# Kernel tuning notes

Measured on AMD Instinct MI355X. Metric: run time of the kernel, lower is better.

## Reference

```python
import jax, jax.numpy as jnp
import numpy as np

B, T, D = 4, 2048, 1024
H = 16
HD = D // H  # 64


def setup_inputs() -> dict:
    key = jax.random.key(0)
    ks = jax.random.split(key, 7)
    scale = 1.0 / np.sqrt(D)
    x = jax.random.normal(ks[0], (B, T, D), dtype=jnp.float32)
    # per-head projection weights, stacked over heads: [H, D, HD]
    Wq = jax.random.normal(ks[1], (H, D, HD), dtype=jnp.float32) * scale
    Wk = jax.random.normal(ks[2], (H, D, HD), dtype=jnp.float32) * scale
    Wv = jax.random.normal(ks[3], (H, D, HD), dtype=jnp.float32) * scale
    s_raw = jnp.zeros((H,), dtype=jnp.float32)  # learnable ssmax scale per head
    proj_W = jax.random.normal(ks[4], (D, D), dtype=jnp.float32) * scale
    proj_b = jax.random.normal(ks[5], (D,), dtype=jnp.float32) * 0.01
    return {"x": x, "Wq": Wq, "Wk": Wk, "Wv": Wv, "s_raw": s_raw,
            "proj_W": proj_W, "proj_b": proj_b}


def reference(x, Wq, Wk, Wv, s_raw, proj_W, proj_b):
    # per-head q/k/v: [B, H, T, HD]
    q = jnp.einsum('btd,hde->bhte', x, Wq)
    k = jnp.einsum('btd,hde->bhte', x, Wk)
    v = jnp.einsum('btd,hde->bhte', x, Wv)

    # ssmax: q scaled by softplus(s) * log(position index, 1-based)
    logn = jnp.log(jnp.arange(1, T + 1, dtype=x.dtype))  # [T]
    s = jax.nn.softplus(s_raw)  # [H]
    q = q * (s[None, :, None, None] * logn[None, None, :, None])

    scores = jnp.einsum('bhte,bhse->bhts', q, k) * (HD ** -0.5)
    causal = jnp.tril(jnp.ones((T, T), dtype=bool))
    scores = jnp.where(causal[None, None], scores, -jnp.inf)
    w = jax.nn.softmax(scores, axis=-1)

    out = jnp.einsum('bhts,bhse->bhte', w, v)          # [B, H, T, HD]
    out = out.transpose(0, 2, 1, 3).reshape(B, T, D)    # concat heads
    return out @ proj_W.T + proj_b
```

## Files before the change

kernel.cpp:

```cpp
#include <hip/hip_runtime.h>
#include <hip/hip_bf16.h>

#define Bv 4
#define Tv 2048
#define Dv 1024
#define Hv 16
#define HDv 64
#define Mv (Bv*Tv)

typedef __hip_bfloat16 bf16;
typedef short s8v __attribute__((ext_vector_type(8)));
typedef float f4v __attribute__((ext_vector_type(4)));
typedef float f16a __attribute__((ext_vector_type(16)));

__device__ __forceinline__ unsigned short f2us(float x){
    bf16 h = __float2bfloat16(x);
    return *reinterpret_cast<unsigned short*>(&h);
}
__device__ __forceinline__ unsigned int pack2(float a, float b){
    return (unsigned int)f2us(a) | ((unsigned int)f2us(b) << 16);
}

__global__ void cvt_kernel(const float* __restrict__ src,
                           unsigned short* __restrict__ dst, int n4) {
    int i = blockIdx.x * 256 + threadIdx.x;
    if (i < n4) {
        float4 f = *(const float4*)(src + (size_t)i * 4);
        ushort4 o;
        o.x = f2us(f.x); o.y = f2us(f.y); o.z = f2us(f.z); o.w = f2us(f.w);
        *(ushort4*)(dst + (size_t)i * 4) = o;
    }
}

__global__ __launch_bounds__(256) void wt_kernel(
    const float* __restrict__ Wq, const float* __restrict__ Wk,
    const float* __restrict__ Wv, unsigned short* __restrict__ Wt)
{
    const int dt  = blockIdx.x;
    const int h   = blockIdx.y;
    const int sel = blockIdx.z;
    const float* W = (sel == 0) ? Wq : ((sel == 1) ? Wk : Wv);
    const float* Wh = W + (size_t)h * Dv * HDv;
    __shared__ float Tf[64][65];
    const int tid = threadIdx.x;
    for (int l = 0; l < 16; ++l) {
        int idx = tid + l * 256;
        int r = idx >> 6, e = idx & 63;
        Tf[r][e] = Wh[(size_t)(dt * 64 + r) * HDv + e];
    }
    __syncthreads();
    unsigned short* out = Wt + ((size_t)sel * Hv + h) * HDv * Dv;
    for (int l = 0; l < 16; ++l) {
        int idx = tid + l * 256;
        int e = idx >> 6, d = idx & 63;
        out[(size_t)e * Dv + dt * 64 + d] = f2us(Tf[d][e]);
    }
}

__global__ __launch_bounds__(256) void qkv_big(
    const unsigned short* __restrict__ xb, const unsigned short* __restrict__ Wc,
    const float* __restrict__ s_raw,
    unsigned short* __restrict__ q, unsigned short* __restrict__ k,
    unsigned short* __restrict__ vT)
{
    const int bm = blockIdx.x;
    const int bn = blockIdx.y;
    const int tid = threadIdx.x;
    const int w = tid >> 6, lane = tid & 63;
    const int n16 = lane & 15, quad = lane >> 4;
    const int wm = w >> 1, wn = w & 1;

    __shared__ __align__(16) unsigned short As[128][72];
    __shared__ __align__(16) unsigned short Bs[128][72];

    f4v acc[4][4];
    f4v zero = {0.f, 0.f, 0.f, 0.f};
    #pragma unroll
    for (int i = 0; i < 4; ++i)
        #pragma unroll
        for (int j = 0; j < 4; ++j) acc[i][j] = zero;

    const int row0 = bm * 128, col0 = bn * 128;

    for (int k0 = 0; k0 < Dv; k0 += 64) {
        __syncthreads();
        #pragma unroll
        for (int l = 0; l < 4; ++l) {
            int idx = tid + l * 256;
            int r = idx >> 3, g = idx & 7;
            *(ulonglong2*)(&As[r][g * 8]) =
                *(const ulonglong2*)(xb + (size_t)(row0 + r) * Dv + k0 + g * 8);
            *(ulonglong2*)(&Bs[r][g * 8]) =
                *(const ulonglong2*)(Wc + (size_t)(col0 + r) * Dv + k0 + g * 8);
        }
        __syncthreads();
        #pragma unroll
        for (int ks = 0; ks < 2; ++ks) {
            s8v bfr[4];
            #pragma unroll
            for (int ni = 0; ni < 4; ++ni)
                bfr[ni] = *(const s8v*)(&Bs[wn * 64 + ni * 16 + n16][ks * 32 + quad * 8]);
            #pragma unroll
            for (int mi = 0; mi < 4; ++mi) {
                s8v afr = *(const s8v*)(&As[wm * 64 + mi * 16 + n16][ks * 32 + quad * 8]);
                #pragma unroll
                for (int ni = 0; ni < 4; ++ni)
                    acc[mi][ni] = __builtin_amdgcn_mfma_f32_16x16x32_bf16(afr, bfr[ni], acc[mi][ni], 0, 0, 0);
            }
        }
    }

    #pragma unroll
    for (int ni = 0; ni < 4; ++ni) {
        int n = col0 + wn * 64 + ni * 16 + n16;
        int sel = n >> 10, h = (n >> 6) & 15, e = n & 63;
        if (sel == 2) {
            #pragma unroll
            for (int mi = 0; mi < 4; ++mi) {
                int row = row0 + wm * 64 + mi * 16 + quad * 4;
                int bb_ = row >> 11, t = row & (Tv - 1);
                ushort4 o4;
                o4.x = f2us(acc[mi][ni][0]); o4.y = f2us(acc[mi][ni][1]);
                o4.z = f2us(acc[mi][ni][2]); o4.w = f2us(acc[mi][ni][3]);
                *(ushort4*)(vT + ((size_t)(bb_ * Hv + h) * HDv + e) * Tv + t) = o4;
            }
        } else {
            unsigned short* out = (sel == 0) ? q : k;
            float sc_h = (sel == 0) ? log1pf(expf(s_raw[h])) * 0.125f : 1.0f;
            #pragma unroll
            for (int mi = 0; mi < 4; ++mi) {
                #pragma unroll
                for (int r = 0; r < 4; ++r) {
                    int row = row0 + wm * 64 + mi * 16 + quad * 4 + r;
                    int bb_ = row >> 11, t = row & (Tv - 1);
                    float rs = (sel == 0) ? sc_h * logf((float)(t + 1)) : 1.0f;
                    out[((size_t)(bb_ * Hv + h) * Tv + t) * HDv + e] = f2us(acc[mi][ni][r] * rs);
                }
            }
        }
    }
}

__global__ __launch_bounds__(256) void attn_mfma(
    const unsigned short* __restrict__ q, const unsigned short* __restrict__ k,
    const unsigned short* __restrict__ vT, unsigned short* __restrict__ attn)
{
    const int qt = (Tv / 128 - 1) - (int)blockIdx.x;
    const int bh = blockIdx.y;
    const int b = bh >> 4, h = bh & 15;
    const int tid = threadIdx.x;
    const int w = tid >> 6, lane = tid & 63;
    const int l31 = lane & 31, hi = lane >> 5;

    __shared__ __align__(16) unsigned short Ks[64][72];
    __shared__ __align__(16) unsigned short VTs[64][72];

    const size_t hb = (size_t)(b * Hv + h) * Tv * HDv;
    const int qstrip = qt * 128 + w * 32;
    const int myq = qstrip + l31;

    s8v qf[4];
    #pragma unroll
    for (int ks = 0; ks < 4; ++ks)
        qf[ks] = *(const s8v*)(q + hb + (size_t)myq * HDv + ks * 16 + hi * 8);

    f16a st0, st1, ot0, ot1;
    #pragma unroll
    for (int i = 0; i < 16; ++i) { ot0[i] = 0.f; ot1[i] = 0.f; }
    float lrun = 0.f;

    const int ktmax = 2 * qt + 1;
    for (int kt = 0; kt <= ktmax; ++kt) {
        const int s0 = kt * 64;
        __syncthreads();
        #pragma unroll
        for (int l = 0; l < 2; ++l) {
            int p = tid + l * 256;
            int r = p >> 3, g = p & 7;
            *(ulonglong2*)(&Ks[r][g * 8]) =
                *(const ulonglong2*)(k + hb + (size_t)(s0 + r) * HDv + g * 8);
            *(ulonglong2*)(&VTs[r][g * 8]) =
                *(const ulonglong2*)(vT + hb + (size_t)r * Tv + s0 + g * 8);
        }
        __syncthreads();
        if (s0 > qstrip + 31) continue;

        #pragma unroll
        for (int i = 0; i < 16; ++i) { st0[i] = 0.f; st1[i] = 0.f; }
        #pragma unroll
        for (int ks = 0; ks < 4; ++ks) {
            s8v a0 = *(const s8v*)(&Ks[l31][ks * 16 + hi * 8]);
            s8v a1 = *(const s8v*)(&Ks[32 + l31][ks * 16 + hi * 8]);
            st0 = __builtin_amdgcn_mfma_f32_32x32x16_bf16(a0, qf[ks], st0, 0, 0, 0);
            st1 = __builtin_amdgcn_mfma_f32_32x32x16_bf16(a1, qf[ks], st1, 0, 0, 0);
        }
        if (s0 + 63 > qstrip) {
            #pragma unroll
            for (int reg = 0; reg < 16; ++reg) {
                int srow = (reg & 3) + 8 * (reg >> 2) + 4 * hi;
                if (s0 + srow > myq)      st0[reg] = -1e30f;
                if (s0 + 32 + srow > myq) st1[reg] = -1e30f;
            }
        }
        float lsum = 0.f;
        #pragma unroll
        for (int i = 0; i < 16; ++i) {
            st0[i] = __expf(st0[i]);
            st1[i] = __expf(st1[i]);
            lsum += st0[i] + st1[i];
        }
        lrun += lsum;

        unsigned int pk[16];
        #pragma unroll
        for (int g = 0; g < 4; ++g) {
            pk[2 * g]         = pack2(st0[4 * g],     st0[4 * g + 1]);
            pk[2 * g + 1]     = pack2(st0[4 * g + 2], st0[4 * g + 3]);
            pk[8 + 2 * g]     = pack2(st1[4 * g],     st1[4 * g + 1]);
            pk[8 + 2 * g + 1] = pack2(st1[4 * g + 2], st1[4 * g + 3]);
        }
        #pragma unroll
        for (int ks = 0; ks < 4; ++ks) {
            int base = (ks >> 1) * 8 + (ks & 1) * 4;
            unsigned int v0 = hi ? pk[base]     : pk[base + 2];
            unsigned int v1 = hi ? pk[base + 1] : pk[base + 3];
            unsigned int r0 = (unsigned int)__shfl_xor((int)v0, 32);
            unsigned int r1 = (unsigned int)__shfl_xor((int)v1, 32);
            union { s8v v; unsigned int d[4]; } bf;
            bf.d[0] = hi ? r0 : pk[base];
            bf.d[1] = hi ? r1 : pk[base + 1];
            bf.d[2] = hi ? pk[base + 2] : r0;
            bf.d[3] = hi ? pk[base + 3] : r1;
            s8v a0 = *(const s8v*)(&VTs[l31][ks * 16 + hi * 8]);
            s8v a1 = *(const s8v*)(&VTs[32 + l31][ks * 16 + hi * 8]);
            ot0 = __builtin_amdgcn_mfma_f32_32x32x16_bf16(a0, bf.v, ot0, 0, 0, 0);
            ot1 = __builtin_amdgcn_mfma_f32_32x32x16_bf16(a1, bf.v, ot1, 0, 0, 0);
        }
    }

    float ltot = lrun + __shfl_xor(lrun, 32);
    float inv = 1.0f / ltot;
    size_t obase = ((size_t)(b * Tv) + myq) * Dv + h * HDv;
    #pragma unroll
    for (int g = 0; g < 4; ++g) {
        ushort4 o4;
        o4.x = f2us(ot0[4 * g]     * inv); o4.y = f2us(ot0[4 * g + 1] * inv);
        o4.z = f2us(ot0[4 * g + 2] * inv); o4.w = f2us(ot0[4 * g + 3] * inv);
        *(ushort4*)(attn + obase + 8 * g + 4 * hi) = o4;
        o4.x = f2us(ot1[4 * g]     * inv); o4.y = f2us(ot1[4 * g + 1] * inv);
        o4.z = f2us(ot1[4 * g + 2] * inv); o4.w = f2us(ot1[4 * g + 3] * inv);
        *(ushort4*)(attn + obase + 32 + 8 * g + 4 * hi) = o4;
    }
}

__global__ __launch_bounds__(256) void proj_big(
    const unsigned short* __restrict__ attn, const unsigned short* __restrict__ Wb,
    const float* __restrict__ bias, float* __restrict__ out)
{
    const int bm = blockIdx.x;
    const int bn = blockIdx.y;
    const int tid = threadIdx.x;
    const int w = tid >> 6, lane = tid & 63;
    const int n16 = lane & 15, quad = lane >> 4;
    const int wm = w >> 1, wn = w & 1;

    __shared__ __align__(16) unsigned short As[128][72];
    __shared__ __align__(16) unsigned short Bs[128][72];

    f4v acc[4][4];
    f4v zero = {0.f, 0.f, 0.f, 0.f};
    #pragma unroll
    for (int i = 0; i < 4; ++i)
        #pragma unroll
        for (int j = 0; j < 4; ++j) acc[i][j] = zero;

    const int row0 = bm * 128, col0 = bn * 128;

    for (int k0 = 0; k0 < Dv; k0 += 64) {
        __syncthreads();
        #pragma unroll
        for (int l = 0; l < 4; ++l) {
            int idx = tid + l * 256;
            int r = idx >> 3, g = idx & 7;
            *(ulonglong2*)(&As[r][g * 8]) =
                *(const ulonglong2*)(attn + (size_t)(row0 + r) * Dv + k0 + g * 8);
            *(ulonglong2*)(&Bs[r][g * 8]) =
                *(const ulonglong2*)(Wb + (size_t)(col0 + r) * Dv + k0 + g * 8);
        }
        __syncthreads();
        #pragma unroll
        for (int ks = 0; ks < 2; ++ks) {
            s8v bfr[4];
            #pragma unroll
            for (int ni = 0; ni < 4; ++ni)
                bfr[ni] = *(const s8v*)(&Bs[wn * 64 + ni * 16 + n16][ks * 32 + quad * 8]);
            #pragma unroll
            for (int mi = 0; mi < 4; ++mi) {
                s8v afr = *(const s8v*)(&As[wm * 64 + mi * 16 + n16][ks * 32 + quad * 8]);
                #pragma unroll
                for (int ni = 0; ni < 4; ++ni)
                    acc[mi][ni] = __builtin_amdgcn_mfma_f32_16x16x32_bf16(afr, bfr[ni], acc[mi][ni], 0, 0, 0);
            }
        }
    }
    #pragma unroll
    for (int ni = 0; ni < 4; ++ni) {
        int n = col0 + wn * 64 + ni * 16 + n16;
        float bn_ = bias[n];
        #pragma unroll
        for (int mi = 0; mi < 4; ++mi) {
            #pragma unroll
            for (int r = 0; r < 4; ++r) {
                int m = row0 + wm * 64 + mi * 16 + quad * 4 + r;
                out[(size_t)m * Dv + n] = acc[mi][ni][r] + bn_;
            }
        }
    }
}

extern "C" void kernel_launch(void* const* d_in, const int* in_sizes, int n_in,
                              void* d_out, int out_size, void* d_ws, size_t ws_size,
                              hipStream_t stream) {
    const float* x     = (const float*)d_in[0];
    const float* Wq    = (const float*)d_in[1];
    const float* Wk    = (const float*)d_in[2];
    const float* Wv    = (const float*)d_in[3];
    const float* s_raw = (const float*)d_in[4];
    const float* projW = (const float*)d_in[5];
    const float* projb = (const float*)d_in[6];
    float* out = (float*)d_out;

    const size_t nx  = (size_t)Mv * Dv;
    const size_t nqk = (size_t)Bv * Hv * Tv * HDv;
    unsigned short* x_bf = (unsigned short*)d_ws;
    unsigned short* qb   = x_bf + nx;
    unsigned short* kb   = qb + nqk;
    unsigned short* vTb  = kb + nqk;
    unsigned short* Wt   = vTb + nqk;
    unsigned short* Wpb  = Wt + (size_t)3 * Hv * HDv * Dv;
    unsigned short* attn = x_bf;

    cvt_kernel<<<(int)(nx / 4 / 256), 256, 0, stream>>>(x, x_bf, (int)(nx / 4));
    cvt_kernel<<<(int)((size_t)Dv * Dv / 4 / 256), 256, 0, stream>>>(projW, Wpb, Dv * Dv / 4);
    wt_kernel<<<dim3(16, 16, 3), 256, 0, stream>>>(Wq, Wk, Wv, Wt);
    qkv_big<<<dim3(Mv / 128, 3072 / 128), 256, 0, stream>>>(x_bf, Wt, s_raw, qb, kb, vTb);
    attn_mfma<<<dim3(Tv / 128, Bv * Hv), 256, 0, stream>>>(qb, kb, vTb, attn);
    proj_big<<<dim3(Mv / 128, Dv / 128), 256, 0, stream>>>(attn, Wpb, projb, out);
}
```

Baseline: 322.0 us.

## Use direct global-to-LDS loads in GEMMs and register-prefetch K/V in attention

```diff
diff --git a/kernel.cpp b/kernel.cpp
--- a/kernel.cpp
+++ b/kernel.cpp
@@ -19,6 +19,11 @@
 }
 __device__ __forceinline__ unsigned int pack2(float a, float b){
     return (unsigned int)f2us(a) | ((unsigned int)f2us(b) << 16);
+}
+__device__ __forceinline__ void glds16(const unsigned short* g, unsigned short* lds_base){
+    __builtin_amdgcn_global_load_lds(
+        (const __attribute__((address_space(1))) unsigned int*)g,
+        (__attribute__((address_space(3))) unsigned int*)lds_base, 16, 0, 0);
 }
 
 __global__ void cvt_kernel(const float* __restrict__ src,
@@ -70,8 +75,8 @@
     const int n16 = lane & 15, quad = lane >> 4;
     const int wm = w >> 1, wn = w & 1;
 
-    __shared__ __align__(16) unsigned short As[128][72];
-    __shared__ __align__(16) unsigned short Bs[128][72];
+    __shared__ __align__(16) unsigned short As[128 * 64];
+    __shared__ __align__(16) unsigned short Bs[128 * 64];
 
     f4v acc[4][4];
     f4v zero = {0.f, 0.f, 0.f, 0.f};
@@ -81,17 +86,15 @@
         for (int j = 0; j < 4; ++j) acc[i][j] = zero;
 
     const int row0 = bm * 128, col0 = bn * 128;
+    const int lr = lane >> 3, lc = (lane & 7) * 8;
 
     for (int k0 = 0; k0 < Dv; k0 += 64) {
         __syncthreads();
         #pragma unroll
-        for (int l = 0; l < 4; ++l) {
-            int idx = tid + l * 256;
-            int r = idx >> 3, g = idx & 7;
-            *(ulonglong2*)(&As[r][g * 8]) =
-                *(const ulonglong2*)(xb + (size_t)(row0 + r) * Dv + k0 + g * 8);
-            *(ulonglong2*)(&Bs[r][g * 8]) =
-                *(const ulonglong2*)(Wc + (size_t)(col0 + r) * Dv + k0 + g * 8);
+        for (int i = 0; i < 4; ++i) {
+            int rb = w * 32 + i * 8;
+            glds16(xb + (size_t)(row0 + rb + lr) * Dv + k0 + lc, &As[rb * 64]);
+            glds16(Wc + (size_t)(col0 + rb + lr) * Dv + k0 + lc, &Bs[rb * 64]);
         }
         __syncthreads();
         #pragma unroll
@@ -99,10 +102,10 @@
             s8v bfr[4];
             #pragma unroll
             for (int ni = 0; ni < 4; ++ni)
-                bfr[ni] = *(const s8v*)(&Bs[wn * 64 + ni * 16 + n16][ks * 32 + quad * 8]);
+                bfr[ni] = *(const s8v*)(&Bs[(wn * 64 + ni * 16 + n16) * 64 + ks * 32 + quad * 8]);
             #pragma unroll
             for (int mi = 0; mi < 4; ++mi) {
-                s8v afr = *(const s8v*)(&As[wm * 64 + mi * 16 + n16][ks * 32 + quad * 8]);
+                s8v afr = *(const s8v*)(&As[(wm * 64 + mi * 16 + n16) * 64 + ks * 32 + quad * 8]);
                 #pragma unroll
                 for (int ni = 0; ni < 4; ++ni)
                     acc[mi][ni] = __builtin_amdgcn_mfma_f32_16x16x32_bf16(afr, bfr[ni], acc[mi][ni], 0, 0, 0);
@@ -169,20 +172,31 @@
     for (int i = 0; i < 16; ++i) { ot0[i] = 0.f; ot1[i] = 0.f; }
     float lrun = 0.f;
 
+    const int r_ = tid >> 3, g_ = (tid & 7) * 8;
+    const int r2 = (tid + 256) >> 3, g2 = (tid & 7) * 8;
+
+    ulonglong2 kr0, kr1, vr0, vr1;
+    kr0 = *(const ulonglong2*)(k + hb + (size_t)r_ * HDv + g_);
+    vr0 = *(const ulonglong2*)(vT + hb + (size_t)r_ * Tv + 0 + g_);
+    kr1 = *(const ulonglong2*)(k + hb + (size_t)r2 * HDv + g2);
+    vr1 = *(const ulonglong2*)(vT + hb + (size_t)r2 * Tv + 0 + g2);
+
     const int ktmax = 2 * qt + 1;
     for (int kt = 0; kt <= ktmax; ++kt) {
         const int s0 = kt * 64;
         __syncthreads();
-        #pragma unroll
-        for (int l = 0; l < 2; ++l) {
-            int p = tid + l * 256;
-            int r = p >> 3, g = p & 7;
-            *(ulonglong2*)(&Ks[r][g * 8]) =
-                *(const ulonglong2*)(k + hb + (size_t)(s0 + r) * HDv + g * 8);
-            *(ulonglong2*)(&VTs[r][g * 8]) =
-                *(const ulonglong2*)(vT + hb + (size_t)r * Tv + s0 + g * 8);
-        }
-        __syncthreads();
+        *(ulonglong2*)(&Ks[r_][g_]) = kr0;
+        *(ulonglong2*)(&VTs[r_][g_]) = vr0;
+        *(ulonglong2*)(&Ks[r2][g2]) = kr1;
+        *(ulonglong2*)(&VTs[r2][g2]) = vr1;
+        __syncthreads();
+        if (kt < ktmax) {
+            const int sn = s0 + 64;
+            kr0 = *(const ulonglong2*)(k + hb + (size_t)(sn + r_) * HDv + g_);
+            vr0 = *(const ulonglong2*)(vT + hb + (size_t)r_ * Tv + sn + g_);
+            kr1 = *(const ulonglong2*)(k + hb + (size_t)(sn + r2) * HDv + g2);
+            vr1 = *(const ulonglong2*)(vT + hb + (size_t)r2 * Tv + sn + g2);
+        }
         if (s0 > qstrip + 31) continue;
 
         #pragma unroll
@@ -264,8 +278,8 @@
     const int n16 = lane & 15, quad = lane >> 4;
     const int wm = w >> 1, wn = w & 1;
 
-    __shared__ __align__(16) unsigned short As[128][72];
-    __shared__ __align__(16) unsigned short Bs[128][72];
+    __shared__ __align__(16) unsigned short As[128 * 64];
+    __shared__ __align__(16) unsigned short Bs[128 * 64];
 
     f4v acc[4][4];
     f4v zero = {0.f, 0.f, 0.f, 0.f};
@@ -275,17 +289,15 @@
         for (int j = 0; j < 4; ++j) acc[i][j] = zero;
 
     const int row0 = bm * 128, col0 = bn * 128;
+    const int lr = lane >> 3, lc = (lane & 7) * 8;
 
     for (int k0 = 0; k0 < Dv; k0 += 64) {
         __syncthreads();
         #pragma unroll
-        for (int l = 0; l < 4; ++l) {
-            int idx = tid + l * 256;
-            int r = idx >> 3, g = idx & 7;
-            *(ulonglong2*)(&As[r][g * 8]) =
-                *(const ulonglong2*)(attn + (size_t)(row0 + r) * Dv + k0 + g * 8);
-            *(ulonglong2*)(&Bs[r][g * 8]) =
-                *(const ulonglong2*)(Wb + (size_t)(col0 + r) * Dv + k0 + g * 8);
+        for (int i = 0; i < 4; ++i) {
+            int rb = w * 32 + i * 8;
+            glds16(attn + (size_t)(row0 + rb + lr) * Dv + k0 + lc, &As[rb * 64]);
+            glds16(Wb   + (size_t)(col0 + rb + lr) * Dv + k0 + lc, &Bs[rb * 64]);
         }
         __syncthreads();
         #pragma unroll
@@ -293,10 +305,10 @@
             s8v bfr[4];
             #pragma unroll
             for (int ni = 0; ni < 4; ++ni)
-                bfr[ni] = *(const s8v*)(&Bs[wn * 64 + ni * 16 + n16][ks * 32 + quad * 8]);
+                bfr[ni] = *(const s8v*)(&Bs[(wn * 64 + ni * 16 + n16) * 64 + ks * 32 + quad * 8]);
             #pragma unroll
             for (int mi = 0; mi < 4; ++mi) {
-                s8v afr = *(const s8v*)(&As[wm * 64 + mi * 16 + n16][ks * 32 + quad * 8]);
+                s8v afr = *(const s8v*)(&As[(wm * 64 + mi * 16 + n16) * 64 + ks * 32 + quad * 8]);
                 #pragma unroll
                 for (int ni = 0; ni < 4; ++ni)
                     acc[mi][ni] = __builtin_amdgcn_mfma_f32_16x16x32_bf16(afr, bfr[ni], acc[mi][ni], 0, 0, 0);
```

Measured after the change: 326.5 us. About the same (+1.4%).
